# Kernel tuning notes

Measured on AMD Instinct MI355X. Metric: run time of the kernel, lower is better.

The kernel has to match this reference:

```python
import jax, jax.numpy as jnp
import numpy as np

B, Z, H, TC, TD, DOUT = 128, 512, 512, 16, 16, 176
DIN_DEC = DOUT + H  # 688: concat(prev_note, conductor_embedding)


def setup_inputs() -> dict:
    key = jax.random.key(0)
    ks = jax.random.split(key, 24)

    def glorot(k, shape):
        lim = np.sqrt(6.0 / (shape[0] + shape[1]))
        return jax.random.uniform(k, shape, jnp.float32, -lim, lim)

    return {
        'z_ssm_embedding': jax.random.normal(ks[0], (B, Z), jnp.float32),
        'pianoroll': jax.random.uniform(ks[1], (B, TC * TD, DOUT), jnp.float32),
        'ssm': jax.random.uniform(ks[2], (B, TC * TD, TC * TD), jnp.float32),
        # z -> conductor initial states (h1,c1,h2,c2), tanh dense
        'Wz': glorot(ks[3], (Z, 4 * H)), 'bz': jnp.zeros((4 * H,), jnp.float32),
        # conductor 2-layer LSTM (input 512)
        'cond_W1': glorot(ks[4], (H, 4 * H)), 'cond_U1': glorot(ks[5], (H, 4 * H)), 'cond_b1': jnp.zeros((4 * H,), jnp.float32),
        'cond_W2': glorot(ks[6], (H, 4 * H)), 'cond_U2': glorot(ks[7], (H, 4 * H)), 'cond_b2': jnp.zeros((4 * H,), jnp.float32),
        # conductor embedding -> decoder initial states, tanh dense
        'Wcd': glorot(ks[8], (H, 4 * H)), 'bcd': jnp.zeros((4 * H,), jnp.float32),
        # core decoder 2-layer LSTM (input 688)
        'dec_W1': glorot(ks[9], (DIN_DEC, 4 * H)), 'dec_U1': glorot(ks[10], (H, 4 * H)), 'dec_b1': jnp.zeros((4 * H,), jnp.float32),
        'dec_W2': glorot(ks[11], (H, 4 * H)), 'dec_U2': glorot(ks[12], (H, 4 * H)), 'dec_b2': jnp.zeros((4 * H,), jnp.float32),
        # output projection (softmax)
        'Wp': glorot(ks[13], (H, DOUT)), 'bp': jnp.zeros((DOUT,), jnp.float32),
    }


def _lstm_step(x, h, c, W, U, b):
    g = x @ W + h @ U + b  # (B, 4H), keras gate order i,f,g,o
    i, f, gg, o = jnp.split(g, 4, axis=-1)
    c = jax.nn.sigmoid(f) * c + jax.nn.sigmoid(i) * jnp.tanh(gg)
    h = jax.nn.sigmoid(o) * jnp.tanh(c)
    return h, c


def reference(z_ssm_embedding, pianoroll, ssm,
              Wz, bz,
              cond_W1, cond_U1, cond_b1, cond_W2, cond_U2, cond_b2,
              Wcd, bcd,
              dec_W1, dec_U1, dec_b1, dec_W2, dec_U2, dec_b2,
              Wp, bp):
    b = z_ssm_embedding.shape[0]
    # conductor initial states from latent (tanh dense, split per layer h/c)
    s = jnp.tanh(z_ssm_embedding @ Wz + bz)
    ch1, cc1, ch2, cc2 = jnp.split(s, 4, axis=-1)
    # In the source, conductor_input and conductor_states are never updated
    # across the outer loop, so the conductor embedding is identical for all
    # 16 segments: compute the single step once.
    x0 = jnp.zeros((b, H), jnp.float32)
    h1, _ = _lstm_step(x0, ch1, cc1, cond_W1, cond_U1, cond_b1)
    cond_emb, _ = _lstm_step(h1, ch2, cc2, cond_W2, cond_U2, cond_b2)  # (B, H)
    # decoder initial states from conductor embedding (same for all segments)
    sd = jnp.tanh(cond_emb @ Wcd + bcd)
    dh1, dc1, dh2, dc2 = jnp.split(sd, 4, axis=-1)

    def seg(note_prev, _):
        def step(carry, _):
            h1, c1, h2, c2, note = carry
            x = jnp.concatenate([note, cond_emb], axis=-1)  # (B, 688)
            h1, c1 = _lstm_step(x, h1, c1, dec_W1, dec_U1, dec_b1)
            h2, c2 = _lstm_step(h1, h2, c2, dec_W2, dec_U2, dec_b2)
            note = jax.nn.softmax(h2 @ Wp + bp, axis=-1)  # output projection
            return (h1, c1, h2, c2, note), note
        (_, _, _, _, note_last), notes = jax.lax.scan(
            step, (dh1, dc1, dh2, dc2, note_prev), None, length=TD)
        return note_last, notes  # notes: (TD, B, DOUT)

    note0 = jnp.zeros((b, DOUT), jnp.float32)
    _, all_notes = jax.lax.scan(seg, note0, None, length=TC)  # (TC, TD, B, DOUT)
    return all_notes.reshape(TC * TD, b, DOUT).transpose(1, 0, 2)  # (B, 256, 176)
```

## Files before the change

### kernel.cpp

```cpp
#include <hip/hip_runtime.h>
#include <hip/hip_bf16.h>
#include <math.h>

#define Bn    128
#define NGn   2048
#define TTn   256
#define DOn   176
#define NBLK  256
#define NTHR  1024
#define HPAR  65536
#define NPAR  24576
#define PLGPOD 98304

typedef unsigned int uint;
using f32x4 = __attribute__((ext_vector_type(4))) float;
using s16x8 = __attribute__((ext_vector_type(8))) short;
union FR { uint u[4]; s16x8 s; };

struct KA {
  const float *z,*Wz,*bz,*cU1,*cb1,*cW2,*cU2,*cb2,*Wcd,*bcd;
  const float *dW1,*dU1,*db1,*dW2,*dU2,*db2,*Wp,*bp;
  float *zT,*sT,*ggate,*h1cT,*ceT,*sdT,*beffP,*db1P,*db2P,*WEp,*plg,*out;
  uint *WAh,*WAl,*WBh,*WBl,*ntpk,*h1pk,*h2pk,*dh1pk,*dh2pk;
};

__device__ unsigned g_cnt_l1[16 * 32];
__device__ unsigned g_cnt;
__device__ unsigned g_gen;
__device__ unsigned pod_leaf[8 * 4 * 32];
__device__ unsigned pod_root[8 * 32];
__device__ unsigned pod_gen[8 * 32];

__device__ __forceinline__ float sigm(float x) { return 1.0f / (1.0f + __expf(-x)); }

__device__ __forceinline__ float aloadF(const float* p) {
  return __hip_atomic_load(p, __ATOMIC_RELAXED, __HIP_MEMORY_SCOPE_AGENT);
}
__device__ __forceinline__ void astoreF(float* p, float v) {
  __hip_atomic_store(p, v, __ATOMIC_RELAXED, __HIP_MEMORY_SCOPE_AGENT);
}
__device__ __forceinline__ uint aloadU(const uint* p) {
  return __hip_atomic_load(p, __ATOMIC_RELAXED, __HIP_MEMORY_SCOPE_AGENT);
}
__device__ __forceinline__ void astoreU(uint* p, uint v) {
  __hip_atomic_store(p, v, __ATOMIC_RELAXED, __HIP_MEMORY_SCOPE_AGENT);
}

__device__ __forceinline__ void split2(float v, unsigned short& h, unsigned short& l) {
  __hip_bfloat16 bh = __float2bfloat16(v);
  float hf = __bfloat162float(bh);
  __hip_bfloat16 bl = __float2bfloat16(v - hf);
  h = *(unsigned short*)&bh; l = *(unsigned short*)&bl;
}
__device__ __forceinline__ uint packsplit(float v) {
  unsigned short h, l; split2(v, h, l);
  return (uint)h | ((uint)l << 16);
}

__device__ __forceinline__ void gbar() {
  __syncthreads();
  if (threadIdx.x == 0) {
    asm volatile("s_waitcnt vmcnt(0)" ::: "memory");
    unsigned g0 = __hip_atomic_load(&g_gen, __ATOMIC_RELAXED, __HIP_MEMORY_SCOPE_AGENT);
    unsigned p1 = __hip_atomic_fetch_add(&g_cnt_l1[(blockIdx.x >> 4) * 32], 1u,
                                         __ATOMIC_RELAXED, __HIP_MEMORY_SCOPE_AGENT);
    if (p1 == 15u) {
      unsigned p2 = __hip_atomic_fetch_add(&g_cnt, 1u, __ATOMIC_RELAXED, __HIP_MEMORY_SCOPE_AGENT);
      if (p2 == 15u) {
        #pragma unroll
        for (int i = 0; i < 16; i++)
          __hip_atomic_store(&g_cnt_l1[i * 32], 0u, __ATOMIC_RELAXED, __HIP_MEMORY_SCOPE_AGENT);
        __hip_atomic_store(&g_cnt, 0u, __ATOMIC_RELAXED, __HIP_MEMORY_SCOPE_AGENT);
        asm volatile("s_waitcnt vmcnt(0)" ::: "memory");
        __hip_atomic_fetch_add(&g_gen, 1u, __ATOMIC_RELAXED, __HIP_MEMORY_SCOPE_AGENT);
      }
    }
    while (__hip_atomic_load(&g_gen, __ATOMIC_RELAXED, __HIP_MEMORY_SCOPE_AGENT) == g0)
      __builtin_amdgcn_s_sleep(1);
  }
  __syncthreads();
}

__device__ __forceinline__ void pbar(int pod, int j) {
  __syncthreads();
  if (threadIdx.x == 0) {
    asm volatile("s_waitcnt vmcnt(0)" ::: "memory");
    unsigned* gen = &pod_gen[pod * 32];
    unsigned g0 = __hip_atomic_load(gen, __ATOMIC_RELAXED, __HIP_MEMORY_SCOPE_AGENT);
    unsigned p = __hip_atomic_fetch_add(&pod_leaf[(pod * 4 + (j >> 3)) * 32], 1u,
                                        __ATOMIC_RELAXED, __HIP_MEMORY_SCOPE_AGENT);
    if (p == 7u) {
      unsigned q = __hip_atomic_fetch_add(&pod_root[pod * 32], 1u,
                                          __ATOMIC_RELAXED, __HIP_MEMORY_SCOPE_AGENT);
      if (q == 3u) {
        #pragma unroll
        for (int l = 0; l < 4; l++)
          __hip_atomic_store(&pod_leaf[(pod * 4 + l) * 32], 0u, __ATOMIC_RELAXED, __HIP_MEMORY_SCOPE_AGENT);
        __hip_atomic_store(&pod_root[pod * 32], 0u, __ATOMIC_RELAXED, __HIP_MEMORY_SCOPE_AGENT);
        asm volatile("s_waitcnt vmcnt(0)" ::: "memory");
        __hip_atomic_fetch_add(gen, 1u, __ATOMIC_RELAXED, __HIP_MEMORY_SCOPE_AGENT);
      }
    }
    while (__hip_atomic_load(gen, __ATOMIC_RELAXED, __HIP_MEMORY_SCOPE_AGENT) == g0) { }
  }
  __syncthreads();
}

__device__ __forceinline__ void stageN(float* __restrict__ xs, const float* __restrict__ X,
                                       int nrows, int b0, int tid) {
  for (int i = tid; i < nrows * 16; i += NTHR)
    xs[i] = aloadF(X + (size_t)(i >> 4) * Bn + b0 + (i & 15));
}

template<int KC>
__device__ __forceinline__ void gemm16(const float* __restrict__ Wb, int colbase,
                                       int kq, int cg, int bg,
                                       const float* __restrict__ xsrc, float acc[16]) {
  const float* wp = Wb + (size_t)(kq * KC) * NGn + colbase + cg * 4;
  const float* xp = xsrc + (kq * KC) * 16 + bg * 4;
  #pragma unroll 2
  for (int kk = 0; kk < KC; kk++) {
    const float4 w4 = *(const float4*)(wp);
    const float4 x4 = *(const float4*)(xp);
    acc[0]  = fmaf(w4.x, x4.x, acc[0]);  acc[1]  = fmaf(w4.x, x4.y, acc[1]);
    acc[2]  = fmaf(w4.x, x4.z, acc[2]);  acc[3]  = fmaf(w4.x, x4.w, acc[3]);
    acc[4]  = fmaf(w4.y, x4.x, acc[4]);  acc[5]  = fmaf(w4.y, x4.y, acc[5]);
    acc[6]  = fmaf(w4.y, x4.z, acc[6]);  acc[7]  = fmaf(w4.y, x4.w, acc[7]);
    acc[8]  = fmaf(w4.z, x4.x, acc[8]);  acc[9]  = fmaf(w4.z, x4.y, acc[9]);
    acc[10] = fmaf(w4.z, x4.z, acc[10]); acc[11] = fmaf(w4.z, x4.w, acc[11]);
    acc[12] = fmaf(w4.w, x4.x, acc[12]); acc[13] = fmaf(w4.w, x4.y, acc[13]);
    acc[14] = fmaf(w4.w, x4.z, acc[14]); acc[15] = fmaf(w4.w, x4.w, acc[15]);
    wp += NGn; xp += 16;
  }
}

__device__ __forceinline__ void pstore(float* __restrict__ part, int kq, int cg, int bg,
                                       const float acc[16]) {
  #pragma unroll
  for (int c = 0; c < 4; c++) {
    float* p = part + (size_t)(kq * 64 + cg * 4 + c) * 17 + bg * 4;
    *(float4*)p = make_float4(acc[c*4], acc[c*4+1], acc[c*4+2], acc[c*4+3]);
  }
}

template<int MODE>
__device__ __forceinline__ void epi_plain(const float* bias, float* out,
                                          int colbase, int b0, int tid,
                                          const float* __restrict__ part) {
  int cl = tid >> 4, bl = tid & 15;
  float s = 0.0f;
  #pragma unroll
  for (int w = 0; w < 8; w++) s += part[(w * 64 + cl) * 17 + bl];
  if (bias) s += bias[colbase + cl];
  if (MODE == 0) s = tanhf(s);
  astoreF(out + (size_t)(colbase + cl) * Bn + b0 + bl, s);
}

__device__ __forceinline__ void cond_nl(const float* gb, const float* cbias,
                                        const float* cin, float* hout, int bid, int tid) {
  int i = bid * NTHR + tid;
  if (i < 512 * Bn) {
    int hid = i >> 7, b = i & 127;
    float gi = aloadF(gb + (size_t)hid * Bn + b)            + cbias[hid];
    float gf = aloadF(gb + (size_t)(512 + hid) * Bn + b)    + cbias[512 + hid];
    float gg = aloadF(gb + (size_t)(1024 + hid) * Bn + b)   + cbias[1024 + hid];
    float go = aloadF(gb + (size_t)(1536 + hid) * Bn + b)   + cbias[1536 + hid];
    float cprev = aloadF(cin + (size_t)hid * Bn + b);
    float c = sigm(gf) * cprev + sigm(gi) * tanhf(gg);
    astoreF(hout + (size_t)hid * Bn + b, sigm(go) * tanhf(c));
  }
}

__device__ __forceinline__ void ldxK(const uint* __restrict__ base, FR& xh, FR& xl) {
  uint w[8];
  #pragma unroll
  for (int e = 0; e < 8; e++) w[e] = aloadU(base + e * 128);
  xh.u[0] = (w[0] & 0xffffu) | (w[1] << 16); xl.u[0] = (w[0] >> 16) | (w[1] & 0xffff0000u);
  xh.u[1] = (w[2] & 0xffffu) | (w[3] << 16); xl.u[1] = (w[2] >> 16) | (w[3] & 0xffff0000u);
  xh.u[2] = (w[4] & 0xffffu) | (w[5] << 16); xl.u[2] = (w[4] >> 16) | (w[5] & 0xffff0000u);
  xh.u[3] = (w[6] & 0xffffu) | (w[7] << 16); xl.u[3] = (w[6] >> 16) | (w[7] & 0xffff0000u);
}

struct MC {
  const uint *WAh,*WAl,*WBh,*WBl,*dh1pk,*dh2pk;
  uint *ntpk,*h1pk,*h2pk;
  const float *beffP,*db2P,*Wp,*bp;
  float *plg;
  float *out;
  float *plog,*gbuf,*cst,*h2s;
  int j, b0;
};

#define MFMA3(ACC, XH, XL, WH, WL)                                            \
  ACC = __builtin_amdgcn_mfma_f32_16x16x32_bf16(XH.s, WH.s, ACC, 0, 0, 0);    \
  ACC = __builtin_amdgcn_mfma_f32_16x16x32_bf16(XL.s, WH.s, ACC, 0, 0, 0);    \
  ACC = __builtin_amdgcn_mfma_f32_16x16x32_bf16(XH.s, WL.s, ACC, 0, 0, 0);

__device__ __forceinline__ void phaseA(const MC& c, int t) {
  const int tid = threadIdx.x, wid = tid >> 6, lane = tid & 63;
  const int m = lane & 15, kh = lane >> 4;
  const int nt = wid & 3, ksq = wid >> 2;
  const int par = t & 1; const bool rst = (t & 15) == 0;
  const int s0 = (ksq == 0) ? 0 : (ksq == 1) ? 6 : (ksq == 2) ? 12 : 17;
  const int s1 = (ksq == 0) ? 6 : (ksq == 1) ? 12 : (ksq == 2) ? 17 : 22;
  const uint* nb = c.ntpk + par * NPAR + kh * 8 * 128 + c.b0 + m;
  const uint* hb = (rst ? c.dh1pk : (c.h1pk + (par ^ 1) * HPAR)) + kh * 8 * 128 + c.b0 + m;
  f32x4 acc = {0.f,0.f,0.f,0.f};
  for (int ks = s0; ks < s1; ks++) {
    FR xh, xl;
    if (ks < 6) ldxK(nb + ks * 32 * 128, xh, xl);
    else        ldxK(hb + (ks * 32 - 192) * 128, xh, xl);
    FR wh, wl;
    *(uint4*)wh.u = *(const uint4*)(c.WAh + (size_t)c.j * 22528 + (ks * 4 + nt) * 256 + lane * 4);
    *(uint4*)wl.u = *(const uint4*)(c.WAl + (size_t)c.j * 22528 + (ks * 4 + nt) * 256 + lane * 4);
    MFMA3(acc, xh, xl, wh, wl)
  }
  #pragma unroll
  for (int r = 0; r < 4; r++) c.plog[((ksq * 4 + nt) * 4 + r) * 64 + lane] = acc[r];
  __syncthreads();
  {
    int cl = tid >> 4, bl = tid & 15;
    float s = 0.f;
    #pragma unroll
    for (int k2 = 0; k2 < 4; k2++)
      s += c.plog[((k2 * 4 + (cl >> 4)) * 4 + (bl & 3)) * 64 + (bl >> 2) * 16 + (cl & 15)];
    c.gbuf[cl * 16 + bl] = s + c.beffP[(size_t)(c.j * 64 + cl) * Bn + c.b0 + bl];
  }
  __syncthreads();
  if (tid < 256) {
    int h = tid >> 4, bl = tid & 15;
    float gi = c.gbuf[(h*4+0)*16+bl], gf = c.gbuf[(h*4+1)*16+bl];
    float gg = c.gbuf[(h*4+2)*16+bl], go = c.gbuf[(h*4+3)*16+bl];
    float cp = rst ? c.cst[512 + tid] : c.cst[tid];
    float cc = sigm(gf) * cp + sigm(gi) * tanhf(gg);
    c.cst[tid] = cc;
    astoreU(c.h1pk + par * HPAR + (size_t)(c.j * 16 + h) * 128 + c.b0 + bl,
            packsplit(sigm(go) * tanhf(cc)));
  }
}

__device__ __forceinline__ void phaseB(const MC& c, int t) {
  const int tid = threadIdx.x, wid = tid >> 6, lane = tid & 63;
  const int m = lane & 15, kh = lane >> 4;
  const int nt = wid & 3, ksq = wid >> 2;
  const int par = t & 1; const bool rst = (t & 15) == 0;
  const uint* s1b = c.h1pk + par * HPAR + kh * 8 * 128 + c.b0 + m;
  const uint* s2b = (rst ? c.dh2pk : (c.h2pk + (par ^ 1) * HPAR)) + kh * 8 * 128 + c.b0 + m;
  f32x4 acc = {0.f,0.f,0.f,0.f};
  #pragma unroll
  for (int kk = 0; kk < 8; kk++) {
    const int ks = ksq * 8 + kk;
    FR xh, xl;
    if (ksq < 2) ldxK(s1b + ks * 32 * 128, xh, xl);
    else         ldxK(s2b + (ks - 16) * 32 * 128, xh, xl);
    FR wh, wl;
    *(uint4*)wh.u = *(const uint4*)(c.WBh + (size_t)c.j * 32768 + (ks * 4 + nt) * 256 + lane * 4);
    *(uint4*)wl.u = *(const uint4*)(c.WBl + (size_t)c.j * 32768 + (ks * 4 + nt) * 256 + lane * 4);
    MFMA3(acc, xh, xl, wh, wl)
  }
  #pragma unroll
  for (int r = 0; r < 4; r++) c.plog[((ksq * 4 + nt) * 4 + r) * 64 + lane] = acc[r];
  __syncthreads();
  {
    int cl = tid >> 4, bl = tid & 15;
    float s = 0.f;
    #pragma unroll
    for (int k2 = 0; k2 < 4; k2++)
      s += c.plog[((k2 * 4 + (cl >> 4)) * 4 + (bl & 3)) * 64 + (bl >> 2) * 16 + (cl & 15)];
    c.gbuf[cl * 16 + bl] = s + c.db2P[c.j * 64 + cl];
  }
  __syncthreads();
  if (tid < 256) {
    int h = tid >> 4, bl = tid & 15;
    float gi = c.gbuf[(h*4+0)*16+bl], gf = c.gbuf[(h*4+1)*16+bl];
    float gg = c.gbuf[(h*4+2)*16+bl], go = c.gbuf[(h*4+3)*16+bl];
    float cp = rst ? c.cst[768 + tid] : c.cst[256 + tid];
    float cc = sigm(gf) * cp + sigm(gi) * tanhf(gg);
    c.cst[256 + tid] = cc;
    float h2v = sigm(go) * tanhf(cc);
    c.h2s[h * 16 + bl] = h2v;
    astoreU(c.h2pk + par * HPAR + (size_t)(c.j * 16 + h) * 128 + c.b0 + bl, packsplit(h2v));
  }
  __syncthreads();
  const int o = tid & 255, q = tid >> 8;
  if (o < DOn) {
    float wv[16];
    #pragma unroll
    for (int h = 0; h < 16; h++) wv[h] = c.Wp[(size_t)(c.j * 16 + h) * DOn + o];
    #pragma unroll
    for (int rep = 0; rep < 4; rep++) {
      const int bl = q * 4 + rep;
      float s = 0.f;
      #pragma unroll
      for (int h = 0; h < 16; h++) s = fmaf(c.h2s[h * 16 + bl], wv[h], s);
      astoreF(c.plg + (size_t)(c.j * 16 + bl) * 192 + o, s);
    }
  }
}

__device__ __forceinline__ void phaseC(const MC& c, int t) {
  if (c.j >= 16) return;
  const int tid = threadIdx.x;
  const int par = t & 1;
  const int b = c.b0 + c.j;
  const int o = tid & 255, q = tid >> 8;
  float s = 0.f;
  if (o < DOn) {
    #pragma unroll
    for (int jj = 0; jj < 8; jj++)
      s += aloadF(c.plg + (size_t)((q * 8 + jj) * 16 + c.j) * 192 + o);
  }
  c.gbuf[q * 256 + o] = s;
  __syncthreads();
  float lg = -1e30f;
  if (tid < 256) {
    float sv = c.gbuf[tid] + c.gbuf[256 + tid] + c.gbuf[512 + tid] + c.gbuf[768 + tid];
    lg = (tid < DOn) ? sv + c.bp[tid] : -1e30f;
    c.plog[tid] = lg;
  }
  __syncthreads();
  for (int st = 128; st > 0; st >>= 1) {
    if (tid < st) c.plog[tid] = fmaxf(c.plog[tid], c.plog[tid + st]);
    __syncthreads();
  }
  const float mx = c.plog[0];
  float e = 0.f;
  if (tid < 256) {
    e = (tid < DOn) ? __expf(lg - mx) : 0.f;
    c.plog[256 + tid] = e;
  }
  __syncthreads();
  for (int st = 128; st > 0; st >>= 1) {
    if (tid < st) c.plog[256 + tid] += c.plog[256 + tid + st];
    __syncthreads();
  }
  const float inv = 1.0f / c.plog[256];
  if (tid < DOn) {
    const float p = e * inv;
    astoreU(c.ntpk + (par ^ 1) * NPAR + tid * 128 + b, packsplit(p));
    c.out[((size_t)b * TTn + t) * DOn + tid] = p;
  }
}

__global__ void __launch_bounds__(NTHR, 1)
hd_kernel(KA A) {
  __shared__ float buf[25088];
  float* xs = buf;
  float* part = buf + 16384;
  const int bid = blockIdx.x, tid = threadIdx.x;
  const int lane = tid & 63;
  const int kqP = tid >> 6, cgP = lane & 15, bgP = lane >> 4;
  const int rP = bid & 31, btP = bid >> 5;
  const int htP = (rP & 7) * 4 + (rP >> 3);
  const int colbaseP = htP * 64, b0P = btP * 16;

  {
    const int i0 = bid * NTHR + tid;
    if (i0 < 512 * Bn) { int zb = i0 >> 9, zk = i0 & 511; astoreF(A.zT + (size_t)zk * Bn + zb, A.z[i0]); }
    if (i0 < NGn) {
      int hid = i0 >> 2, g = i0 & 3, sc = g * 512 + hid;
      astoreF(A.db1P + i0, A.db1[sc]);
      astoreF(A.db2P + i0, A.db2[sc]);
    }
    if (i0 < NPAR) astoreU(A.ntpk + i0, 0u);
    if (i0 < 2048) astoreU(A.ntpk + NPAR + 176 * 128 + i0, 0u);
    for (int i = i0; i < 512 * NGn; i += NBLK * NTHR) {
      int k = i >> 11, pc = i & 2047;
      int hid = pc >> 2, g = pc & 3;
      astoreF(A.WEp + i, A.dW1[(size_t)(176 + k) * NGn + g * 512 + hid]);
    }
    for (int i = i0; i < 720896; i += NBLK * NTHR) {
      int col = i & 2047, kp = i >> 11, k = kp * 2;
      float w0, w1;
      if (k < 176)      { w0 = A.dW1[(size_t)k * NGn + col];       w1 = A.dW1[(size_t)(k + 1) * NGn + col]; }
      else if (k < 192) { w0 = 0.f; w1 = 0.f; }
      else              { w0 = A.dU1[(size_t)(k - 192) * NGn + col]; w1 = A.dU1[(size_t)(k - 191) * NGn + col]; }
      unsigned short h0, l0, h1, l1; split2(w0, h0, l0); split2(w1, h1, l1);
      int g = col >> 9, hid = col & 511;
      int jj = hid >> 4, cl = (hid & 15) * 4 + g;
      int nt = cl >> 4, n = cl & 15;
      int ks = k >> 5, kr = k & 31, lh = kr >> 3, q = (kr >> 1) & 3;
      int idx = ((jj * 22 + ks) * 4 + nt) * 256 + (lh * 16 + n) * 4 + q;
      astoreU(A.WAh + idx, (uint)h0 | ((uint)h1 << 16));
      astoreU(A.WAl + idx, (uint)l0 | ((uint)l1 << 16));
    }
  }
  gbar();
  {
    stageN(xs, A.zT, 512, b0P, tid); __syncthreads();
    if (tid < 512) {
      float acc[16] = {0,0,0,0,0,0,0,0,0,0,0,0,0,0,0,0};
      gemm16<64>(A.Wz, colbaseP, kqP, cgP, bgP, xs, acc);
      pstore(part, kqP, cgP, bgP, acc);
    }
    __syncthreads();
    epi_plain<0>(A.bz, A.sT, colbaseP, b0P, tid, part);
  }
  gbar();
  {
    stageN(xs, A.sT, 512, b0P, tid); __syncthreads();
    if (tid < 512) {
      float acc[16] = {0,0,0,0,0,0,0,0,0,0,0,0,0,0,0,0};
      gemm16<64>(A.cU1, colbaseP, kqP, cgP, bgP, xs, acc);
      pstore(part, kqP, cgP, bgP, acc);
    }
    __syncthreads();
    epi_plain<1>(nullptr, A.ggate, colbaseP, b0P, tid, part);
  }
  gbar();
  cond_nl(A.ggate, A.cb1, A.sT + (size_t)512 * Bn, A.h1cT, bid, tid);
  gbar();
  {
    stageN(xs, A.h1cT, 512, b0P, tid);
    stageN(xs + 8192, A.sT + (size_t)1024 * Bn, 512, b0P, tid);
    __syncthreads();
    if (tid < 512) {
      float acc[16] = {0,0,0,0,0,0,0,0,0,0,0,0,0,0,0,0};
      gemm16<64>(A.cW2, colbaseP, kqP, cgP, bgP, xs, acc);
      gemm16<64>(A.cU2, colbaseP, kqP, cgP, bgP, xs + 8192, acc);
      pstore(part, kqP, cgP, bgP, acc);
    }
    __syncthreads();
    epi_plain<1>(nullptr, A.ggate, colbaseP, b0P, tid, part);
  }
  gbar();
  cond_nl(A.ggate, A.cb2, A.sT + (size_t)1536 * Bn, A.ceT, bid, tid);
  gbar();
  {
    stageN(xs, A.ceT, 512, b0P, tid); __syncthreads();
    if (tid < 512) {
      float acc[16] = {0,0,0,0,0,0,0,0,0,0,0,0,0,0,0,0};
      gemm16<64>(A.Wcd, colbaseP, kqP, cgP, bgP, xs, acc);
      pstore(part, kqP, cgP, bgP, acc);
    }
    __syncthreads();
    epi_plain<0>(A.bcd, A.sdT, colbaseP, b0P, tid, part);
    __syncthreads();
    if (tid < 512) {
      float acc[16] = {0,0,0,0,0,0,0,0,0,0,0,0,0,0,0,0};
      gemm16<64>(A.WEp, colbaseP, kqP, cgP, bgP, xs, acc);
      pstore(part, kqP, cgP, bgP, acc);
    }
    __syncthreads();
    epi_plain<1>(A.db1P, A.beffP, colbaseP, b0P, tid, part);
  }
  gbar();
  {
    const int i0 = bid * NTHR + tid;
    for (int i = i0; i < 1048576; i += NBLK * NTHR) {
      int col = i & 2047, kp = i >> 11, k = kp * 2;
      float w0, w1;
      if (k < 512) { w0 = A.dW2[(size_t)k * NGn + col];         w1 = A.dW2[(size_t)(k + 1) * NGn + col]; }
      else         { w0 = A.dU2[(size_t)(k - 512) * NGn + col]; w1 = A.dU2[(size_t)(k - 511) * NGn + col]; }
      unsigned short h0, l0, h1, l1; split2(w0, h0, l0); split2(w1, h1, l1);
      int g = col >> 9, hid = col & 511;
      int jj = hid >> 4, cl = (hid & 15) * 4 + g;
      int nt = cl >> 4, n = cl & 15;
      int ks = k >> 5, kr = k & 31, lh = kr >> 3, q = (kr >> 1) & 3;
      int idx = ((jj * 32 + ks) * 4 + nt) * 256 + (lh * 16 + n) * 4 + q;
      astoreU(A.WBh + idx, (uint)h0 | ((uint)h1 << 16));
      astoreU(A.WBl + idx, (uint)l0 | ((uint)l1 << 16));
    }
    if (i0 < 512 * Bn) {
      int hid = i0 >> 7, b = i0 & 127;
      astoreU(A.dh1pk + hid * 128 + b, packsplit(aloadF(A.sdT + (size_t)hid * Bn + b)));
      astoreU(A.dh2pk + hid * 128 + b, packsplit(aloadF(A.sdT + (size_t)(1024 + hid) * Bn + b)));
    }
  }
  gbar();

  MC c;
  c.WAh = A.WAh; c.WAl = A.WAl; c.WBh = A.WBh; c.WBl = A.WBl;
  c.dh1pk = A.dh1pk; c.dh2pk = A.dh2pk;
  c.ntpk = A.ntpk; c.h1pk = A.h1pk; c.h2pk = A.h2pk;
  c.beffP = A.beffP; c.db2P = A.db2P; c.Wp = A.Wp; c.bp = A.bp; c.out = A.out;
  c.plog = buf; c.gbuf = buf + 4096; c.cst = buf + 5120; c.h2s = buf + 6144;
  c.j = bid & 31;
  const int pod = bid >> 5;
  c.b0 = pod * 16;
  c.plg = A.plg + (size_t)pod * PLGPOD;
  if (tid < 256) {
    int h = tid >> 4, bl = tid & 15;
    c.cst[512 + tid] = aloadF(A.sdT + (size_t)(512 + c.j * 16 + h) * Bn + c.b0 + bl);
    c.cst[768 + tid] = aloadF(A.sdT + (size_t)(1536 + c.j * 16 + h) * Bn + c.b0 + bl);
  }
  __syncthreads();

  for (int t = 0; t < TTn; t++) {
    phaseA(c, t);
    pbar(pod, c.j);
    phaseB(c, t);
    pbar(pod, c.j);
    phaseC(c, t);
    pbar(pod, c.j);
  }
}

extern "C" void kernel_launch(void* const* d_in, const int* in_sizes, int n_in,
                              void* d_out, int out_size, void* d_ws, size_t ws_size,
                              hipStream_t stream) {
  (void)in_sizes; (void)n_in; (void)out_size; (void)ws_size;
  KA a;
  a.z   = (const float*)d_in[0];
  a.Wz  = (const float*)d_in[3];  a.bz  = (const float*)d_in[4];
  a.cU1 = (const float*)d_in[6];  a.cb1 = (const float*)d_in[7];
  a.cW2 = (const float*)d_in[8];  a.cU2 = (const float*)d_in[9];  a.cb2 = (const float*)d_in[10];
  a.Wcd = (const float*)d_in[11]; a.bcd = (const float*)d_in[12];
  a.dW1 = (const float*)d_in[13]; a.dU1 = (const float*)d_in[14]; a.db1 = (const float*)d_in[15];
  a.dW2 = (const float*)d_in[16]; a.dU2 = (const float*)d_in[17]; a.db2 = (const float*)d_in[18];
  a.Wp  = (const float*)d_in[19]; a.bp  = (const float*)d_in[20];

  float* ws = (float*)d_ws;
  size_t off = 0;
  a.zT    = ws + off; off += (size_t)512  * Bn;
  a.sT    = ws + off; off += (size_t)NGn  * Bn;
  a.ggate = ws + off; off += (size_t)NGn  * Bn;
  a.h1cT  = ws + off; off += (size_t)512  * Bn;
  a.ceT   = ws + off; off += (size_t)512  * Bn;
  a.sdT   = ws + off; off += (size_t)NGn  * Bn;
  a.beffP = ws + off; off += (size_t)NGn  * Bn;
  a.db1P  = ws + off; off += (size_t)NGn;
  a.db2P  = ws + off; off += (size_t)NGn;
  a.WEp   = ws + off; off += (size_t)512 * NGn;
  a.WBh   = (uint*)a.WEp;
  a.WBl   = (uint*)(ws + off); off += (size_t)1048576;
  a.WAh   = (uint*)(ws + off); off += (size_t)720896;
  a.WAl   = (uint*)(ws + off); off += (size_t)720896;
  a.ntpk  = (uint*)(ws + off); off += (size_t)2 * NPAR;
  a.h1pk  = (uint*)(ws + off); off += (size_t)2 * HPAR;
  a.h2pk  = (uint*)(ws + off); off += (size_t)2 * HPAR;
  a.dh1pk = (uint*)(ws + off); off += (size_t)HPAR;
  a.dh2pk = (uint*)(ws + off); off += (size_t)HPAR;
  a.plg   = ws + off; off += (size_t)8 * PLGPOD;
  a.out   = (float*)d_out;

  hd_kernel<<<dim3(NBLK), dim3(NTHR), 0, stream>>>(a);
}
```

Before: 8.477 ms.

## Stage packed recurrent activations in padded LDS and reuse across waves

Before each MFMA phase, the block's 16-batch slice of the packed note, h1 and h2 activation vectors is copied from global memory into shared memory, padded to a row stride of 17 to avoid bank conflicts. The MFMA loops then read their operand fragments from shared memory instead of issuing strided global loads, and each fragment is reused by the four waves that cover the different gate column tiles. The h2 state is staged during phase A so phase B can consume it, and the h1 staged in phase B is reused by the next step's phase A. This adds staging work, an extra barrier per phase and a larger shared-memory footprint, in exchange for fewer redundant global/L2 reads on the serial critical path.

```diff
diff --git a/kernel.cpp b/kernel.cpp
--- a/kernel.cpp
+++ b/kernel.cpp
@@ -171,10 +171,10 @@
   }
 }
 
-__device__ __forceinline__ void ldxK(const uint* __restrict__ base, FR& xh, FR& xl) {
+__device__ __forceinline__ void ldxL17(const uint* __restrict__ p, FR& xh, FR& xl) {
   uint w[8];
   #pragma unroll
-  for (int e = 0; e < 8; e++) w[e] = aloadU(base + e * 128);
+  for (int e = 0; e < 8; e++) w[e] = p[e * 17];
   xh.u[0] = (w[0] & 0xffffu) | (w[1] << 16); xl.u[0] = (w[0] >> 16) | (w[1] & 0xffff0000u);
   xh.u[1] = (w[2] & 0xffffu) | (w[3] << 16); xl.u[1] = (w[2] >> 16) | (w[3] & 0xffff0000u);
   xh.u[2] = (w[4] & 0xffffu) | (w[5] << 16); xl.u[2] = (w[4] >> 16) | (w[5] & 0xffff0000u);
@@ -187,6 +187,7 @@
   const float *beffP,*db2P,*Wp,*bp;
   float *plg;
   float *out;
+  uint *SBu,*NTu;
   float *plog,*gbuf,*cst,*h2s;
   int j, b0;
 };
@@ -195,21 +196,42 @@
   ACC = __builtin_amdgcn_mfma_f32_16x16x32_bf16(XH.s, WH.s, ACC, 0, 0, 0);    \
   ACC = __builtin_amdgcn_mfma_f32_16x16x32_bf16(XL.s, WH.s, ACC, 0, 0, 0);    \
   ACC = __builtin_amdgcn_mfma_f32_16x16x32_bf16(XH.s, WL.s, ACC, 0, 0, 0);
+
+__device__ __forceinline__ void stageSB16(uint* __restrict__ SBu, int r0,
+                                          const uint* __restrict__ src, int b0, int tid) {
+  #pragma unroll
+  for (int rep = 0; rep < 8; rep++) {
+    int idx = tid + rep * NTHR;
+    int k = idx >> 4, bl = idx & 15;
+    SBu[(r0 + k) * 17 + bl] = aloadU(src + k * 128 + b0 + bl);
+  }
+}
+__device__ __forceinline__ void stageNT16(uint* __restrict__ NTu,
+                                          const uint* __restrict__ src, int b0, int tid) {
+  #pragma unroll
+  for (int rep = 0; rep < 3; rep++) {
+    int idx = tid + rep * NTHR;
+    int k = idx >> 4, bl = idx & 15;
+    NTu[k * 17 + bl] = aloadU(src + k * 128 + b0 + bl);
+  }
+}
 
 __device__ __forceinline__ void phaseA(const MC& c, int t) {
   const int tid = threadIdx.x, wid = tid >> 6, lane = tid & 63;
   const int m = lane & 15, kh = lane >> 4;
   const int nt = wid & 3, ksq = wid >> 2;
   const int par = t & 1; const bool rst = (t & 15) == 0;
+  stageNT16(c.NTu, c.ntpk + par * NPAR, c.b0, tid);
+  stageSB16(c.SBu, 512, rst ? c.dh2pk : (c.h2pk + (par ^ 1) * HPAR), c.b0, tid);
+  if (rst) stageSB16(c.SBu, 0, c.dh1pk, c.b0, tid);
+  __syncthreads();
   const int s0 = (ksq == 0) ? 0 : (ksq == 1) ? 6 : (ksq == 2) ? 12 : 17;
   const int s1 = (ksq == 0) ? 6 : (ksq == 1) ? 12 : (ksq == 2) ? 17 : 22;
-  const uint* nb = c.ntpk + par * NPAR + kh * 8 * 128 + c.b0 + m;
-  const uint* hb = (rst ? c.dh1pk : (c.h1pk + (par ^ 1) * HPAR)) + kh * 8 * 128 + c.b0 + m;
   f32x4 acc = {0.f,0.f,0.f,0.f};
   for (int ks = s0; ks < s1; ks++) {
-    FR xh, xl;
-    if (ks < 6) ldxK(nb + ks * 32 * 128, xh, xl);
-    else        ldxK(hb + (ks * 32 - 192) * 128, xh, xl);
+    const uint* xp = (ks < 6) ? (c.NTu + (ks * 32 + kh * 8) * 17 + m)
+                              : (c.SBu + ((ks - 6) * 32 + kh * 8) * 17 + m);
+    FR xh, xl; ldxL17(xp, xh, xl);
     FR wh, wl;
     *(uint4*)wh.u = *(const uint4*)(c.WAh + (size_t)c.j * 22528 + (ks * 4 + nt) * 256 + lane * 4);
     *(uint4*)wl.u = *(const uint4*)(c.WAl + (size_t)c.j * 22528 + (ks * 4 + nt) * 256 + lane * 4);
@@ -244,15 +266,14 @@
   const int m = lane & 15, kh = lane >> 4;
   const int nt = wid & 3, ksq = wid >> 2;
   const int par = t & 1; const bool rst = (t & 15) == 0;
-  const uint* s1b = c.h1pk + par * HPAR + kh * 8 * 128 + c.b0 + m;
-  const uint* s2b = (rst ? c.dh2pk : (c.h2pk + (par ^ 1) * HPAR)) + kh * 8 * 128 + c.b0 + m;
+  stageSB16(c.SBu, 0, c.h1pk + par * HPAR, c.b0, tid);
+  __syncthreads();
   f32x4 acc = {0.f,0.f,0.f,0.f};
   #pragma unroll
   for (int kk = 0; kk < 8; kk++) {
     const int ks = ksq * 8 + kk;
-    FR xh, xl;
-    if (ksq < 2) ldxK(s1b + ks * 32 * 128, xh, xl);
-    else         ldxK(s2b + (ks - 16) * 32 * 128, xh, xl);
+    const uint* xp = c.SBu + (ks * 32 + kh * 8) * 17 + m;
+    FR xh, xl; ldxL17(xp, xh, xl);
     FR wh, wl;
     *(uint4*)wh.u = *(const uint4*)(c.WBh + (size_t)c.j * 32768 + (ks * 4 + nt) * 256 + lane * 4);
     *(uint4*)wl.u = *(const uint4*)(c.WBl + (size_t)c.j * 32768 + (ks * 4 + nt) * 256 + lane * 4);
@@ -327,14 +348,14 @@
   float e = 0.f;
   if (tid < 256) {
     e = (tid < DOn) ? __expf(lg - mx) : 0.f;
-    c.plog[256 + tid] = e;
+    c.plog[260 + tid] = e;
   }
   __syncthreads();
   for (int st = 128; st > 0; st >>= 1) {
-    if (tid < st) c.plog[256 + tid] += c.plog[256 + tid + st];
-    __syncthreads();
-  }
-  const float inv = 1.0f / c.plog[256];
+    if (tid < st) c.plog[260 + tid] += c.plog[260 + tid + st];
+    __syncthreads();
+  }
+  const float inv = 1.0f / c.plog[260];
   if (tid < DOn) {
     const float p = e * inv;
     astoreU(c.ntpk + (par ^ 1) * NPAR + tid * 128 + b, packsplit(p));
@@ -344,7 +365,7 @@
 
 __global__ void __launch_bounds__(NTHR, 1)
 hd_kernel(KA A) {
-  __shared__ float buf[25088];
+  __shared__ float buf[27072];
   float* xs = buf;
   float* part = buf + 16384;
   const int bid = blockIdx.x, tid = threadIdx.x;
@@ -474,7 +495,12 @@
   c.dh1pk = A.dh1pk; c.dh2pk = A.dh2pk;
   c.ntpk = A.ntpk; c.h1pk = A.h1pk; c.h2pk = A.h2pk;
   c.beffP = A.beffP; c.db2P = A.db2P; c.Wp = A.Wp; c.bp = A.bp; c.out = A.out;
-  c.plog = buf; c.gbuf = buf + 4096; c.cst = buf + 5120; c.h2s = buf + 6144;
+  c.SBu = (uint*)buf;
+  c.NTu = (uint*)(buf + 17408);
+  c.plog = buf + 20672;
+  c.gbuf = buf + 24768;
+  c.cst  = buf + 25792;
+  c.h2s  = buf + 26816;
   c.j = bid & 31;
   const int pod = bid >> 5;
   c.b0 = pod * 16;
```

New measurement: 9.403 ms. 1.11x slower.

## Fuse softmax into next step via fixed-point atomic logits, drop a pod barrier

Applied to the files above, without the earlier changes.

Output-projection partial logits are now accumulated with integer atomic adds in fixed point (scale 2^20) into a double-buffered per-pod array, instead of being written to a partial buffer and reduced in a separate phase. Every block then recomputes the softmax for all 16 batch rows of its pod at the start of the next step, one wave per row, and keeps the packed note in LDS. This removes phaseC and one pod barrier per timestep, and replaces the tree barrier with a single monotonic counter. The trade-offs are redundant softmax work in every block, atomic contention, and a loss of precision from fixed-point quantization of the logits.

```diff
diff --git a/kernel.cpp b/kernel.cpp
--- a/kernel.cpp
+++ b/kernel.cpp
@@ -9,8 +9,7 @@
 #define NBLK  256
 #define NTHR  1024
 #define HPAR  65536
-#define NPAR  24576
-#define PLGPOD 98304
+#define ACC_PAR 24576
 
 typedef unsigned int uint;
 using f32x4 = __attribute__((ext_vector_type(4))) float;
@@ -20,16 +19,15 @@
 struct KA {
   const float *z,*Wz,*bz,*cU1,*cb1,*cW2,*cU2,*cb2,*Wcd,*bcd;
   const float *dW1,*dU1,*db1,*dW2,*dU2,*db2,*Wp,*bp;
-  float *zT,*sT,*ggate,*h1cT,*ceT,*sdT,*beffP,*db1P,*db2P,*WEp,*plg,*out;
-  uint *WAh,*WAl,*WBh,*WBl,*ntpk,*h1pk,*h2pk,*dh1pk,*dh2pk;
+  float *zT,*sT,*ggate,*h1cT,*ceT,*sdT,*beffP,*db1P,*db2P,*WEp,*out;
+  uint *WAh,*WAl,*WBh,*WBl,*h1pk,*h2pk,*dh1pk,*dh2pk;
+  int  *accI;
 };
 
 __device__ unsigned g_cnt_l1[16 * 32];
 __device__ unsigned g_cnt;
 __device__ unsigned g_gen;
-__device__ unsigned pod_leaf[8 * 4 * 32];
-__device__ unsigned pod_root[8 * 32];
-__device__ unsigned pod_gen[8 * 32];
+__device__ unsigned pod_ctr[8 * 64];
 
 __device__ __forceinline__ float sigm(float x) { return 1.0f / (1.0f + __expf(-x)); }
 
@@ -44,6 +42,9 @@
 }
 __device__ __forceinline__ void astoreU(uint* p, uint v) {
   __hip_atomic_store(p, v, __ATOMIC_RELAXED, __HIP_MEMORY_SCOPE_AGENT);
+}
+__device__ __forceinline__ int aloadI(const int* p) {
+  return __hip_atomic_load(p, __ATOMIC_RELAXED, __HIP_MEMORY_SCOPE_AGENT);
 }
 
 __device__ __forceinline__ void split2(float v, unsigned short& h, unsigned short& l) {
@@ -81,29 +82,16 @@
   __syncthreads();
 }
 
-__device__ __forceinline__ void pbar(int pod, int j) {
+__device__ __forceinline__ void pbar2(int pod, unsigned& tgt) {
   __syncthreads();
   if (threadIdx.x == 0) {
     asm volatile("s_waitcnt vmcnt(0)" ::: "memory");
-    unsigned* gen = &pod_gen[pod * 32];
-    unsigned g0 = __hip_atomic_load(gen, __ATOMIC_RELAXED, __HIP_MEMORY_SCOPE_AGENT);
-    unsigned p = __hip_atomic_fetch_add(&pod_leaf[(pod * 4 + (j >> 3)) * 32], 1u,
-                                        __ATOMIC_RELAXED, __HIP_MEMORY_SCOPE_AGENT);
-    if (p == 7u) {
-      unsigned q = __hip_atomic_fetch_add(&pod_root[pod * 32], 1u,
-                                          __ATOMIC_RELAXED, __HIP_MEMORY_SCOPE_AGENT);
-      if (q == 3u) {
-        #pragma unroll
-        for (int l = 0; l < 4; l++)
-          __hip_atomic_store(&pod_leaf[(pod * 4 + l) * 32], 0u, __ATOMIC_RELAXED, __HIP_MEMORY_SCOPE_AGENT);
-        __hip_atomic_store(&pod_root[pod * 32], 0u, __ATOMIC_RELAXED, __HIP_MEMORY_SCOPE_AGENT);
-        asm volatile("s_waitcnt vmcnt(0)" ::: "memory");
-        __hip_atomic_fetch_add(gen, 1u, __ATOMIC_RELAXED, __HIP_MEMORY_SCOPE_AGENT);
-      }
-    }
-    while (__hip_atomic_load(gen, __ATOMIC_RELAXED, __HIP_MEMORY_SCOPE_AGENT) == g0) { }
-  }
-  __syncthreads();
+    unsigned* ctr = &pod_ctr[pod * 64];
+    __hip_atomic_fetch_add(ctr, 1u, __ATOMIC_RELAXED, __HIP_MEMORY_SCOPE_AGENT);
+    while ((int)(__hip_atomic_load(ctr, __ATOMIC_RELAXED, __HIP_MEMORY_SCOPE_AGENT) - tgt) < 0) { }
+  }
+  __syncthreads();
+  tgt += 32;
 }
 
 __device__ __forceinline__ void stageN(float* __restrict__ xs, const float* __restrict__ X,
@@ -180,13 +168,23 @@
   xh.u[2] = (w[4] & 0xffffu) | (w[5] << 16); xl.u[2] = (w[4] >> 16) | (w[5] & 0xffff0000u);
   xh.u[3] = (w[6] & 0xffffu) | (w[7] << 16); xl.u[3] = (w[6] >> 16) | (w[7] & 0xffff0000u);
 }
+__device__ __forceinline__ void ldxL17(const uint* __restrict__ p, FR& xh, FR& xl) {
+  uint w[8];
+  #pragma unroll
+  for (int e = 0; e < 8; e++) w[e] = p[e * 17];
+  xh.u[0] = (w[0] & 0xffffu) | (w[1] << 16); xl.u[0] = (w[0] >> 16) | (w[1] & 0xffff0000u);
+  xh.u[1] = (w[2] & 0xffffu) | (w[3] << 16); xl.u[1] = (w[2] >> 16) | (w[3] & 0xffff0000u);
+  xh.u[2] = (w[4] & 0xffffu) | (w[5] << 16); xl.u[2] = (w[4] >> 16) | (w[5] & 0xffff0000u);
+  xh.u[3] = (w[6] & 0xffffu) | (w[7] << 16); xl.u[3] = (w[6] >> 16) | (w[7] & 0xffff0000u);
+}
 
 struct MC {
   const uint *WAh,*WAl,*WBh,*WBl,*dh1pk,*dh2pk;
-  uint *ntpk,*h1pk,*h2pk;
+  uint *h1pk,*h2pk;
   const float *beffP,*db2P,*Wp,*bp;
-  float *plg;
+  int *accI;
   float *out;
+  uint *NTu;
   float *plog,*gbuf,*cst,*h2s;
   int j, b0;
 };
@@ -196,19 +194,51 @@
   ACC = __builtin_amdgcn_mfma_f32_16x16x32_bf16(XL.s, WH.s, ACC, 0, 0, 0);    \
   ACC = __builtin_amdgcn_mfma_f32_16x16x32_bf16(XH.s, WL.s, ACC, 0, 0, 0);
 
-__device__ __forceinline__ void phaseA(const MC& c, int t) {
+__device__ __forceinline__ void phaseA(const MC& c, int t, bool doLSTM) {
   const int tid = threadIdx.x, wid = tid >> 6, lane = tid & 63;
   const int m = lane & 15, kh = lane >> 4;
+  const int par = t & 1; const bool rst = (t & 15) == 0;
+  if (t > 0) {
+    const int wv = wid;
+    const int* ai = c.accI + ((par ^ 1) * ACC_PAR) + wv * 192;
+    float lg[3], pv[3];
+    #pragma unroll
+    for (int rep = 0; rep < 3; rep++) {
+      int o = lane + rep * 64;
+      lg[rep] = (o < DOn) ? (float)aloadI(ai + o) * (1.0f / 1048576.0f) + c.bp[o] : -1e30f;
+    }
+    float mx = fmaxf(fmaxf(lg[0], lg[1]), lg[2]);
+    #pragma unroll
+    for (int d = 1; d < 64; d <<= 1) mx = fmaxf(mx, __shfl_xor(mx, d));
+    float sum = 0.f;
+    #pragma unroll
+    for (int rep = 0; rep < 3; rep++) {
+      int o = lane + rep * 64;
+      pv[rep] = (o < DOn) ? __expf(lg[rep] - mx) : 0.f;
+      sum += pv[rep];
+    }
+    #pragma unroll
+    for (int d = 1; d < 64; d <<= 1) sum += __shfl_xor(sum, d);
+    const float inv = 1.0f / sum;
+    #pragma unroll
+    for (int rep = 0; rep < 3; rep++) {
+      int o = lane + rep * 64;
+      float p = pv[rep] * inv;
+      c.NTu[o * 17 + wv] = (o < DOn) ? packsplit(p) : 0u;
+      if (c.j < 16 && wv == c.j && o < DOn)
+        c.out[((size_t)(c.b0 + c.j) * TTn + (t - 1)) * DOn + o] = p;
+    }
+  }
+  __syncthreads();
+  if (!doLSTM) return;
   const int nt = wid & 3, ksq = wid >> 2;
-  const int par = t & 1; const bool rst = (t & 15) == 0;
   const int s0 = (ksq == 0) ? 0 : (ksq == 1) ? 6 : (ksq == 2) ? 12 : 17;
   const int s1 = (ksq == 0) ? 6 : (ksq == 1) ? 12 : (ksq == 2) ? 17 : 22;
-  const uint* nb = c.ntpk + par * NPAR + kh * 8 * 128 + c.b0 + m;
   const uint* hb = (rst ? c.dh1pk : (c.h1pk + (par ^ 1) * HPAR)) + kh * 8 * 128 + c.b0 + m;
   f32x4 acc = {0.f,0.f,0.f,0.f};
   for (int ks = s0; ks < s1; ks++) {
     FR xh, xl;
-    if (ks < 6) ldxK(nb + ks * 32 * 128, xh, xl);
+    if (ks < 6) ldxL17(c.NTu + (ks * 32 + kh * 8) * 17 + m, xh, xl);
     else        ldxK(hb + (ks * 32 - 192) * 128, xh, xl);
     FR wh, wl;
     *(uint4*)wh.u = *(const uint4*)(c.WAh + (size_t)c.j * 22528 + (ks * 4 + nt) * 256 + lane * 4);
@@ -293,53 +323,13 @@
       float s = 0.f;
       #pragma unroll
       for (int h = 0; h < 16; h++) s = fmaf(c.h2s[h * 16 + bl], wv[h], s);
-      astoreF(c.plg + (size_t)(c.j * 16 + bl) * 192 + o, s);
-    }
-  }
-}
-
-__device__ __forceinline__ void phaseC(const MC& c, int t) {
-  if (c.j >= 16) return;
-  const int tid = threadIdx.x;
-  const int par = t & 1;
-  const int b = c.b0 + c.j;
-  const int o = tid & 255, q = tid >> 8;
-  float s = 0.f;
-  if (o < DOn) {
-    #pragma unroll
-    for (int jj = 0; jj < 8; jj++)
-      s += aloadF(c.plg + (size_t)((q * 8 + jj) * 16 + c.j) * 192 + o);
-  }
-  c.gbuf[q * 256 + o] = s;
-  __syncthreads();
-  float lg = -1e30f;
-  if (tid < 256) {
-    float sv = c.gbuf[tid] + c.gbuf[256 + tid] + c.gbuf[512 + tid] + c.gbuf[768 + tid];
-    lg = (tid < DOn) ? sv + c.bp[tid] : -1e30f;
-    c.plog[tid] = lg;
-  }
-  __syncthreads();
-  for (int st = 128; st > 0; st >>= 1) {
-    if (tid < st) c.plog[tid] = fmaxf(c.plog[tid], c.plog[tid + st]);
-    __syncthreads();
-  }
-  const float mx = c.plog[0];
-  float e = 0.f;
-  if (tid < 256) {
-    e = (tid < DOn) ? __expf(lg - mx) : 0.f;
-    c.plog[256 + tid] = e;
-  }
-  __syncthreads();
-  for (int st = 128; st > 0; st >>= 1) {
-    if (tid < st) c.plog[256 + tid] += c.plog[256 + tid + st];
-    __syncthreads();
-  }
-  const float inv = 1.0f / c.plog[256];
-  if (tid < DOn) {
-    const float p = e * inv;
-    astoreU(c.ntpk + (par ^ 1) * NPAR + tid * 128 + b, packsplit(p));
-    c.out[((size_t)b * TTn + t) * DOn + tid] = p;
-  }
+      __hip_atomic_fetch_add(c.accI + par * ACC_PAR + bl * 192 + o,
+                             __float2int_rn(s * 1048576.0f),
+                             __ATOMIC_RELAXED, __HIP_MEMORY_SCOPE_AGENT);
+    }
+  }
+  if (tid < 96)
+    astoreU((uint*)(c.accI + (par ^ 1) * ACC_PAR + c.j * 96 + tid), 0u);
 }
 
 __global__ void __launch_bounds__(NTHR, 1)
@@ -353,6 +343,10 @@
   const int rP = bid & 31, btP = bid >> 5;
   const int htP = (rP & 7) * 4 + (rP >> 3);
   const int colbaseP = htP * 64, b0P = btP * 16;
+  const int pod = bid >> 5;
+
+  unsigned tgt = __hip_atomic_load(&pod_ctr[pod * 64], __ATOMIC_RELAXED,
+                                   __HIP_MEMORY_SCOPE_AGENT) + 32;
 
   {
     const int i0 = bid * NTHR + tid;
@@ -362,8 +356,7 @@
       astoreF(A.db1P + i0, A.db1[sc]);
       astoreF(A.db2P + i0, A.db2[sc]);
     }
-    if (i0 < NPAR) astoreU(A.ntpk + i0, 0u);
-    if (i0 < 2048) astoreU(A.ntpk + NPAR + 176 * 128 + i0, 0u);
+    if (i0 < 2 * ACC_PAR) astoreU((uint*)(A.accI + i0), 0u);
     for (int i = i0; i < 512 * NGn; i += NBLK * NTHR) {
       int k = i >> 11, pc = i & 2047;
       int hid = pc >> 2, g = pc & 3;
@@ -472,28 +465,31 @@
   MC c;
   c.WAh = A.WAh; c.WAl = A.WAl; c.WBh = A.WBh; c.WBl = A.WBl;
   c.dh1pk = A.dh1pk; c.dh2pk = A.dh2pk;
-  c.ntpk = A.ntpk; c.h1pk = A.h1pk; c.h2pk = A.h2pk;
+  c.h1pk = A.h1pk; c.h2pk = A.h2pk;
   c.beffP = A.beffP; c.db2P = A.db2P; c.Wp = A.Wp; c.bp = A.bp; c.out = A.out;
-  c.plog = buf; c.gbuf = buf + 4096; c.cst = buf + 5120; c.h2s = buf + 6144;
+  c.accI = A.accI + pod * 3072;
+  c.NTu = (uint*)buf;
+  c.plog = buf + 3264;
+  c.gbuf = buf + 7360;
+  c.cst  = buf + 8384;
+  c.h2s  = buf + 9408;
   c.j = bid & 31;
-  const int pod = bid >> 5;
   c.b0 = pod * 16;
-  c.plg = A.plg + (size_t)pod * PLGPOD;
   if (tid < 256) {
     int h = tid >> 4, bl = tid & 15;
     c.cst[512 + tid] = aloadF(A.sdT + (size_t)(512 + c.j * 16 + h) * Bn + c.b0 + bl);
     c.cst[768 + tid] = aloadF(A.sdT + (size_t)(1536 + c.j * 16 + h) * Bn + c.b0 + bl);
   }
+  for (int i = tid; i < 3264; i += NTHR) c.NTu[i] = 0u;
   __syncthreads();
 
   for (int t = 0; t < TTn; t++) {
-    phaseA(c, t);
-    pbar(pod, c.j);
+    phaseA(c, t, true);
+    pbar2(pod, tgt);
     phaseB(c, t);
-    pbar(pod, c.j);
-    phaseC(c, t);
-    pbar(pod, c.j);
-  }
+    pbar2(pod, tgt);
+  }
+  phaseA(c, TTn, false);
 }
 
 extern "C" void kernel_launch(void* const* d_in, const int* in_sizes, int n_in,
@@ -526,12 +522,11 @@
   a.WBl   = (uint*)(ws + off); off += (size_t)1048576;
   a.WAh   = (uint*)(ws + off); off += (size_t)720896;
   a.WAl   = (uint*)(ws + off); off += (size_t)720896;
-  a.ntpk  = (uint*)(ws + off); off += (size_t)2 * NPAR;
   a.h1pk  = (uint*)(ws + off); off += (size_t)2 * HPAR;
   a.h2pk  = (uint*)(ws + off); off += (size_t)2 * HPAR;
   a.dh1pk = (uint*)(ws + off); off += (size_t)HPAR;
   a.dh2pk = (uint*)(ws + off); off += (size_t)HPAR;
-  a.plg   = ws + off; off += (size_t)8 * PLGPOD;
+  a.accI  = (int*)(ws + off);  off += (size_t)2 * ACC_PAR;
   a.out   = (float*)d_out;
 
   hd_kernel<<<dim3(NBLK), dim3(NTHR), 0, stream>>>(a);
```

Measured after the change: 7.773 ms. 8.3% less time.
